# Kernel optimization log

Measured on AMD Instinct MI355X. Metric: run time of the kernel, lower is better.

The kernel has to match this reference:

```python
import jax, jax.numpy as jnp
import numpy as np

EPS_NORM = 1e-6
EPS_Q = 1e-5


def rmsnorm(x, g):
    ms = jnp.mean(x * x, axis=-1, keepdims=True)
    return x * jax.lax.rsqrt(ms + EPS_NORM) * g


def bitlinear(x, w, g):
    # RMSNorm -> absmax int8 activation quant -> absmean ternary weight quant -> matmul -> rescale
    xn = rmsnorm(x, g)
    x_scale = jnp.maximum(jnp.max(jnp.abs(xn), axis=-1, keepdims=True), EPS_Q)
    xq = jnp.clip(jnp.round(xn * 127.0 / x_scale), -128.0, 127.0)  # STE irrelevant in fwd
    w_scale = jnp.maximum(jnp.mean(jnp.abs(w)), EPS_Q)
    wq = jnp.clip(jnp.round(w / w_scale), -1.0, 1.0)
    out = jnp.einsum('btd,od->bto', xq, wq)
    return out * (w_scale * x_scale / 127.0)


def rotate_half(x):
    d = x.shape[-1] // 2
    return jnp.concatenate([-x[..., d:], x[..., :d]], axis=-1)


def apply_rope(x, cos, sin):
    # x: [B, H, T, D]; cos/sin: [T, D]
    return x * cos[None, None] + rotate_half(x) * sin[None, None]


def setup_inputs() -> dict:
    key = jax.random.key(0)
    ks = jax.random.split(key, 12)
    B, T, D, H, KV = 2, 2048, 2048, 32, 8
    hd = D // H
    bound = 1.0 / np.sqrt(D)  # ~ kaiming_uniform fan_in
    inp = {
        'x': jax.random.normal(ks[0], (B, T, D), jnp.float32),
        'cos': jax.random.uniform(ks[1], (T, hd), jnp.float32),
        'sin': jax.random.uniform(ks[2], (T, hd), jnp.float32),
        'wq': jax.random.uniform(ks[3], (H * hd, D), jnp.float32, -bound, bound),
        'wk': jax.random.uniform(ks[4], (KV * hd, D), jnp.float32, -bound, bound),
        'wv': jax.random.uniform(ks[5], (KV * hd, D), jnp.float32, -bound, bound),
        'wo': jax.random.uniform(ks[6], (D, H * hd), jnp.float32, -bound, bound),
        'gq': jnp.ones((D,), jnp.float32),
        'gk': jnp.ones((D,), jnp.float32),
        'gv': jnp.ones((D,), jnp.float32),
        'go': jnp.ones((H * hd,), jnp.float32),
    }
    return inp


def reference(x, cos, sin, wq, wk, wv, wo, gq, gk, gv, go):
    B, T, D = x.shape
    H, KV = 32, 8
    hd = D // H
    n_rep = H // KV

    q = bitlinear(x, wq, gq).reshape(B, T, H, hd).transpose(0, 2, 1, 3)   # [B,H,T,hd]
    k = bitlinear(x, wk, gk).reshape(B, T, KV, hd).transpose(0, 2, 1, 3)  # [B,KV,T,hd]
    v = bitlinear(x, wv, gv).reshape(B, T, KV, hd).transpose(0, 2, 1, 3)

    q = apply_rope(q, cos, sin)
    k = apply_rope(k, cos, sin)

    # GQA repeat_interleave on head dim
    k = jnp.repeat(k, n_rep, axis=1)  # [B,H,T,hd]
    v = jnp.repeat(v, n_rep, axis=1)

    scale = 1.0 / np.sqrt(hd)
    scores = jnp.einsum('bhqd,bhkd->bhqk', q, k) * scale
    causal = jnp.tril(jnp.ones((T, T), bool))
    scores = jnp.where(causal, scores, jnp.finfo(scores.dtype).min)
    attn = jax.nn.softmax(scores, axis=-1)
    out = jnp.einsum('bhqk,bhkd->bhqd', attn, v)
    out = out.transpose(0, 2, 1, 3).reshape(B, T, H * hd)
    return bitlinear(out, wo, go)
```

## Files before the change

### kernel.cpp

```cpp
#include <hip/hip_runtime.h>
#include <stdint.h>

constexpr int B   = 2;
constexpr int T   = 2048;
constexpr int D   = 2048;
constexpr int H   = 32;
constexpr int KVH = 8;
constexpr int HD  = 64;
constexpr int R   = B * T;
constexpr int OKV = KVH * HD;

using bf16x8 = __attribute__((ext_vector_type(8))) __bf16;
using f32x4  = __attribute__((ext_vector_type(4))) float;
using i32x4  = __attribute__((ext_vector_type(4))) int;

__device__ inline float fast_exp2(float x) {
#if __has_builtin(__builtin_amdgcn_exp2f)
    return __builtin_amdgcn_exp2f(x);
#else
    return exp2f(x);
#endif
}

__device__ inline float max3f(float a, float b, float c) {
    return fmaxf(fmaxf(a, b), c);
}

__device__ inline uint16_t f2bf(float f) {
    uint32_t u = __float_as_uint(f);
    u += 0x7fff + ((u >> 16) & 1);
    return (uint16_t)(u >> 16);
}

__device__ inline uint32_t pack_bf16(float a, float b) {
#if __has_builtin(__builtin_amdgcn_cvt_pk_bf16_f32)
    union { __attribute__((ext_vector_type(2))) __bf16 v; uint32_t u; } r;
    r.v = __builtin_amdgcn_cvt_pk_bf16_f32(a, b);
    return r.u;
#else
    return (uint32_t)f2bf(a) | ((uint32_t)f2bf(b) << 16);
#endif
}

__device__ inline void async16(const void* g, void* l) {
    __builtin_amdgcn_global_load_lds((const __attribute__((address_space(1))) unsigned int*)g,
                                     (__attribute__((address_space(3))) unsigned int*)l,
                                     16, 0, 0);
}

__global__ void absmean4_kernel(const float* __restrict__ w0, const float* __restrict__ w1,
                                const float* __restrict__ w2, const float* __restrict__ w3,
                                double* __restrict__ sums) {
    __shared__ float red[256];
    const float* ws[4] = {w0, w1, w2, w3};
    const int ns[4] = {D * D, OKV * D, OKV * D, D * D};
    int wi = blockIdx.y;
    const float* w = ws[wi];
    int n = ns[wi];
    int tid = threadIdx.x;
    float s = 0.f;
    for (int i = blockIdx.x * 256 + tid; i < n; i += gridDim.x * 256)
        s += fabsf(w[i]);
    red[tid] = s;
    __syncthreads();
    for (int st = 128; st > 0; st >>= 1) {
        if (tid < st) red[tid] += red[tid + st];
        __syncthreads();
    }
    if (tid == 0) atomicAdd(&sums[wi], (double)red[0]);
}

__global__ void quantw4_kernel(const float* __restrict__ w0, const float* __restrict__ w1,
                               const float* __restrict__ w2, const float* __restrict__ w3,
                               int8_t* __restrict__ o0, int8_t* __restrict__ o1,
                               int8_t* __restrict__ o2, int8_t* __restrict__ o3,
                               const double* __restrict__ sums) {
    const float* ws[4] = {w0, w1, w2, w3};
    int8_t* os[4] = {o0, o1, o2, o3};
    const int ns[4] = {D * D, OKV * D, OKV * D, D * D};
    int wi = blockIdx.y;
    const float* w = ws[wi];
    int8_t* o = os[wi];
    int n = ns[wi];
    float wsc = fmaxf((float)(sums[wi] / (double)n), 1e-5f);
    for (int i = blockIdx.x * 256 + threadIdx.x; i < n; i += gridDim.x * 256) {
        float q = rintf(w[i] / wsc);
        q = fminf(fmaxf(q, -1.f), 1.f);
        o[i] = (int8_t)q;
    }
}

__global__ __launch_bounds__(256) void rmsq3_kernel(const float* __restrict__ X,
        const float* __restrict__ g0, const float* __restrict__ g1, const float* __restrict__ g2,
        int8_t* __restrict__ o0, int8_t* __restrict__ o1, int8_t* __restrict__ o2,
        float* __restrict__ s0, float* __restrict__ s1, float* __restrict__ s2) {
    __shared__ float red[256];
    int row = blockIdx.x, tid = threadIdx.x;
    const float* xr = X + (size_t)row * D;
    float xv[8];
    float ss = 0.f;
#pragma unroll
    for (int i = 0; i < 8; i++) { xv[i] = xr[tid + 256 * i]; ss += xv[i] * xv[i]; }
    red[tid] = ss;
    __syncthreads();
    for (int st = 128; st > 0; st >>= 1) {
        if (tid < st) red[tid] += red[tid + st];
        __syncthreads();
    }
    float rstd = 1.0f / sqrtf(red[0] / (float)D + 1e-6f);

    const float* gs[3] = {g0, g1, g2};
    int8_t* os[3] = {o0, o1, o2};
    float* sc[3] = {s0, s1, s2};
#pragma unroll
    for (int v = 0; v < 3; v++) {
        float xn[8];
        float amax = 0.f;
#pragma unroll
        for (int i = 0; i < 8; i++) {
            xn[i] = xv[i] * rstd * gs[v][tid + 256 * i];
            amax = fmaxf(amax, fabsf(xn[i]));
        }
        __syncthreads();
        red[tid] = amax;
        __syncthreads();
        for (int st = 128; st > 0; st >>= 1) {
            if (tid < st) red[tid] = fmaxf(red[tid], red[tid + st]);
            __syncthreads();
        }
        float xsv = fmaxf(red[0], 1e-5f);
        float q127 = 127.0f / xsv;
#pragma unroll
        for (int i = 0; i < 8; i++) {
            float q = rintf(xn[i] * q127);
            q = fminf(fmaxf(q, -128.f), 127.f);
            os[v][(size_t)row * D + tid + 256 * i] = (int8_t)q;
        }
        if (tid == 0) sc[v][row] = xsv;
    }
}

__global__ __launch_bounds__(256) void rmsq_kernel(const float* __restrict__ X,
                                                   const float* __restrict__ g,
                                                   int8_t* __restrict__ Xq,
                                                   float* __restrict__ xs_out) {
    __shared__ float red[256];
    int row = blockIdx.x, tid = threadIdx.x;
    const float* xr = X + (size_t)row * D;
    float xv[8];
    float ss = 0.f;
#pragma unroll
    for (int i = 0; i < 8; i++) { xv[i] = xr[tid + 256 * i]; ss += xv[i] * xv[i]; }
    red[tid] = ss;
    __syncthreads();
    for (int st = 128; st > 0; st >>= 1) {
        if (tid < st) red[tid] += red[tid + st];
        __syncthreads();
    }
    float rstd = 1.0f / sqrtf(red[0] / (float)D + 1e-6f);

    float xn[8];
    float amax = 0.f;
#pragma unroll
    for (int i = 0; i < 8; i++) {
        xn[i] = xv[i] * rstd * g[tid + 256 * i];
        amax = fmaxf(amax, fabsf(xn[i]));
    }
    __syncthreads();
    red[tid] = amax;
    __syncthreads();
    for (int st = 128; st > 0; st >>= 1) {
        if (tid < st) red[tid] = fmaxf(red[tid], red[tid + st]);
        __syncthreads();
    }
    float xs = fmaxf(red[0], 1e-5f);
    float q127 = 127.0f / xs;
#pragma unroll
    for (int i = 0; i < 8; i++) {
        float q = rintf(xn[i] * q127);
        q = fminf(fmaxf(q, -128.f), 127.f);
        Xq[(size_t)row * D + tid + 256 * i] = (int8_t)q;
    }
    if (tid == 0) xs_out[row] = xs;
}

template<int BN, int MODE>
__global__ __launch_bounds__(512, 4) void gemm_i8_mfma(const int8_t* __restrict__ Xq,
                                                       const int8_t* __restrict__ W8,
                                                       void* __restrict__ outp,
                                                       const float* __restrict__ xs,
                                                       const double* __restrict__ wsum, int wi,
                                                       int nw, int O,
                                                       const float* __restrict__ cs,
                                                       const float* __restrict__ sn) {
    constexpr int NT = BN / 16;
    __shared__ __align__(16) uint8_t As[2][128 * 128];
    __shared__ __align__(16) uint8_t Bs[2][BN * 128];

    const int tid  = threadIdx.x;
    const int lane = tid & 63;
    const int wv   = tid >> 6;
    const int n    = lane & 15, quad = lane >> 4;
    const int row0 = blockIdx.y * 128;
    const int col0 = blockIdx.x * BN;

    i32x4 acc[NT] = {};

    auto stage = [&](int k0, int buf) {
#pragma unroll
        for (int ps = 0; ps < 2; ps++) {
            int p = ps * 512 + wv * 64 + lane;
            int r = p >> 3, s = p & 7;
            int c = s ^ (r & 7);
            async16(Xq + (size_t)(row0 + r) * D + k0 + c * 16,
                    &As[buf][(ps * 512 + wv * 64) * 16]);
        }
#pragma unroll
        for (int ps = 0; ps < BN / 64; ps++) {
            int p = ps * 512 + wv * 64 + lane;
            int r = p >> 3, s = p & 7;
            int c = s ^ (r & 7);
            async16(W8 + (size_t)(col0 + r) * D + k0 + c * 16,
                    &Bs[buf][(ps * 512 + wv * 64) * 16]);
        }
    };

    stage(0, 0);
    __syncthreads();

    for (int k0 = 0; k0 < D; k0 += 128) {
        const int cur = (k0 >> 7) & 1;
        if (k0 + 128 < D) stage(k0 + 128, cur ^ 1);
#pragma unroll
        for (int t = 0; t < 2; t++) {
            int r = wv * 16 + n;
            i32x4 af = *(const i32x4*)&As[cur][r * 128 + (((t * 4 + quad) ^ (r & 7)) * 16)];
            i32x4 bfr[NT];
#pragma unroll
            for (int nt = 0; nt < NT; nt++) {
                int rb = nt * 16 + n;
                bfr[nt] = *(const i32x4*)&Bs[cur][rb * 128 + (((t * 4 + quad) ^ (rb & 7)) * 16)];
            }
#pragma unroll
            for (int nt = 0; nt < NT; nt++)
                acc[nt] = __builtin_amdgcn_mfma_i32_16x16x64_i8(af, bfr[nt], acc[nt], 0, 0, 0);
        }
        __syncthreads();
    }

    float w = fmaxf((float)(wsum[wi] / (double)nw), 1e-5f);
#pragma unroll
    for (int r2 = 0; r2 < 4; r2++) {
        int row = row0 + wv * 16 + quad * 4 + r2;
        float f = w * xs[row] * (1.0f / 127.0f);
        if (MODE == 0) {
            float* out = (float*)outp;
#pragma unroll
            for (int nt = 0; nt < NT; nt++)
                out[(size_t)row * O + col0 + nt * 16 + n] = (float)acc[nt][r2] * f;
        } else {
            uint16_t* out = (uint16_t*)outp;
            int t = row & (T - 1);
#pragma unroll
            for (int nt = 0; nt < NT; nt++) {
                if ((nt & 3) >= 2) continue;
                int i = (nt * 16 + n) & 63;
                float a  = (float)acc[nt][r2] * f;
                float bb = (float)acc[nt + 2][r2] * f;
                float c0 = cs[t * HD + i],      s0 = sn[t * HD + i];
                float c1 = cs[t * HD + i + 32], s1 = sn[t * HD + i + 32];
                out[(size_t)row * O + col0 + nt * 16 + n]       = f2bf(a * c0 - bb * s0);
                out[(size_t)row * O + col0 + (nt + 2) * 16 + n] = f2bf(bb * c1 + a * s1);
            }
        }
    }
}

__global__ __launch_bounds__(512, 4) void gemm_kv_mfma(const int8_t* __restrict__ Xv,
                                                       const int8_t* __restrict__ Xk,
                                                       const int8_t* __restrict__ Wv8,
                                                       const int8_t* __restrict__ Wk8,
                                                       uint16_t* __restrict__ vt,
                                                       uint16_t* __restrict__ kout,
                                                       const float* __restrict__ xsv,
                                                       const float* __restrict__ xsk,
                                                       const double* __restrict__ wsum,
                                                       const float* __restrict__ cs,
                                                       const float* __restrict__ sn) {
    constexpr int BN = 64, NT = 4;
    __shared__ __align__(16) uint8_t As[2][128 * 128];
    __shared__ __align__(16) uint8_t Bs[2][BN * 128];

    const int z = blockIdx.z;
    const int8_t* Xq = z ? Xk : Xv;
    const int8_t* W8 = z ? Wk8 : Wv8;
    const float* xs  = z ? xsk : xsv;

    const int tid  = threadIdx.x;
    const int lane = tid & 63;
    const int wv   = tid >> 6;
    const int n    = lane & 15, quad = lane >> 4;
    const int row0 = blockIdx.y * 128;
    const int col0 = blockIdx.x * BN;

    i32x4 acc[NT] = {};

    auto stage = [&](int k0, int buf) {
#pragma unroll
        for (int ps = 0; ps < 2; ps++) {
            int p = ps * 512 + wv * 64 + lane;
            int r = p >> 3, s = p & 7;
            int c = s ^ (r & 7);
            async16(Xq + (size_t)(row0 + r) * D + k0 + c * 16,
                    &As[buf][(ps * 512 + wv * 64) * 16]);
        }
        {
            int p = wv * 64 + lane;
            int r = p >> 3, s = p & 7;
            int c = s ^ (r & 7);
            async16(W8 + (size_t)(col0 + r) * D + k0 + c * 16,
                    &Bs[buf][(wv * 64) * 16]);
        }
    };

    stage(0, 0);
    __syncthreads();

    for (int k0 = 0; k0 < D; k0 += 128) {
        const int cur = (k0 >> 7) & 1;
        if (k0 + 128 < D) stage(k0 + 128, cur ^ 1);
#pragma unroll
        for (int t = 0; t < 2; t++) {
            int r = wv * 16 + n;
            i32x4 af = *(const i32x4*)&As[cur][r * 128 + (((t * 4 + quad) ^ (r & 7)) * 16)];
            i32x4 bfr[NT];
#pragma unroll
            for (int nt = 0; nt < NT; nt++) {
                int rb = nt * 16 + n;
                bfr[nt] = *(const i32x4*)&Bs[cur][rb * 128 + (((t * 4 + quad) ^ (rb & 7)) * 16)];
            }
#pragma unroll
            for (int nt = 0; nt < NT; nt++)
                acc[nt] = __builtin_amdgcn_mfma_i32_16x16x64_i8(af, bfr[nt], acc[nt], 0, 0, 0);
        }
        __syncthreads();
    }

    float w = fmaxf((float)(wsum[z ? 1 : 2] / (double)(OKV * D)), 1e-5f);
    if (z == 0) {
        int rowb = row0 + wv * 16 + quad * 4;
        int bb = rowb >> 11;
        int tb = rowb & (T - 1);
        float fr[4];
#pragma unroll
        for (int r2 = 0; r2 < 4; r2++)
            fr[r2] = w * xs[rowb + r2] * (1.0f / 127.0f);
#pragma unroll
        for (int nt = 0; nt < NT; nt++) {
            int col = col0 + nt * 16 + n;
            int kvh = col >> 6, d = col & 63;
            uint2 w2;
            w2.x = pack_bf16((float)acc[nt][0] * fr[0], (float)acc[nt][1] * fr[1]);
            w2.y = pack_bf16((float)acc[nt][2] * fr[2], (float)acc[nt][3] * fr[3]);
            *(uint2*)(vt + ((size_t)(bb * KVH + kvh) * 64 + d) * T + tb) = w2;
        }
    } else {
#pragma unroll
        for (int r2 = 0; r2 < 4; r2++) {
            int row = row0 + wv * 16 + quad * 4 + r2;
            float f = w * xs[row] * (1.0f / 127.0f);
            int t = row & (T - 1);
#pragma unroll
            for (int nt = 0; nt < 2; nt++) {
                int i = (nt * 16 + n) & 63;
                float a  = (float)acc[nt][r2] * f;
                float bb = (float)acc[nt + 2][r2] * f;
                float c0 = cs[t * HD + i],      s0 = sn[t * HD + i];
                float c1 = cs[t * HD + i + 32], s1 = sn[t * HD + i + 32];
                kout[(size_t)row * OKV + col0 + nt * 16 + n]       = f2bf(a * c0 - bb * s0);
                kout[(size_t)row * OKV + col0 + (nt + 2) * 16 + n] = f2bf(bb * c1 + a * s1);
            }
        }
    }
}

__global__ __launch_bounds__(512, 4) void attn_mfma_kernel(const uint16_t* __restrict__ qh,
                                                           const uint16_t* __restrict__ kh,
                                                           const uint16_t* __restrict__ vt,
                                                           float* __restrict__ out) {
    __shared__ __align__(16) uint16_t KsB[2][64 * 64];
    __shared__ __align__(16) uint16_t VtB[2][64 * 64];
    __shared__ __align__(16) uint16_t Pw[8][16 * 72];

    const int tid  = threadIdx.x;
    const int lane = tid & 63;
    const int wv   = tid >> 6;
    const int p = blockIdx.x, h = blockIdx.y, b = blockIdx.z;
    const int kvh = h >> 2;
    const int n = lane & 15, quad = lane >> 4;
    const float SC = 0.125f * 1.44269504089f;
    const float DEFER = 44.3614f;

    int q_lo[2] = { p * 128 + wv * 16, (15 - p) * 128 + wv * 16 };

    bf16x8 qf[2][2];
#pragma unroll
    for (int i = 0; i < 2; i++) {
        const uint16_t* qp = qh + (size_t)(b * T + q_lo[i] + n) * D + h * HD + quad * 8;
        qf[i][0] = *(const bf16x8*)(qp);
        qf[i][1] = *(const bf16x8*)(qp + 32);
    }

    f32x4 o[2][4] = {};
    float ls[2] = { 0.f, 0.f };
    float m[2] = { -INFINITY, -INFINITY };

    const uint16_t* kbase = kh + (size_t)b * T * OKV + kvh * HD;
    const uint16_t* vbase = vt + (size_t)(b * KVH + kvh) * 64 * T;

    const int nch = 32 - 2 * p;

    {
        int r = tid >> 3, sl = tid & 7;
        int c = sl ^ (r & 7);
        async16(kbase + (size_t)r * OKV + c * 8, &KsB[0][wv * 512]);
        async16(vbase + (size_t)r * T + c * 8,   &VtB[0][wv * 512]);
    }
    __syncthreads();

    for (int ch = 0; ch < nch; ch++) {
        const int cur = ch & 1;
        if (ch + 1 < nch) {
            const int t1 = (ch + 1) * 64;
            int r = tid >> 3, sl = tid & 7;
            int c = sl ^ (r & 7);
            async16(kbase + (size_t)(t1 + r) * OKV + c * 8, &KsB[cur ^ 1][wv * 512]);
            async16(vbase + (size_t)r * T + t1 + c * 8,     &VtB[cur ^ 1][wv * 512]);
        }
        const int t0 = ch * 64;
        const uint16_t* Ks = KsB[cur];
        const uint16_t* Vs = VtB[cur];

#pragma unroll
        for (int i = 0; i < 2; i++) {
            if (t0 > q_lo[i] + 15) continue;
            f32x4 sv[4] = {};
            __builtin_amdgcn_s_setprio(1);
#pragma unroll
            for (int ks = 0; ks < 2; ks++)
#pragma unroll
                for (int mt = 0; mt < 4; mt++) {
                    int r = mt * 16 + n;
                    bf16x8 kfr = *(const bf16x8*)&Ks[r * 64 + (((ks * 4 + quad) ^ (n & 7)) * 8)];
                    sv[mt] = __builtin_amdgcn_mfma_f32_16x16x32_bf16(kfr, qf[i][ks], sv[mt], 0, 0, 0);
                }
            __builtin_amdgcn_s_setprio(0);

            const int qg = q_lo[i] + n;
            const bool diag = (t0 + 63 > q_lo[i]);
            if (diag) {
#pragma unroll
                for (int mt = 0; mt < 4; mt++)
#pragma unroll
                    for (int r2 = 0; r2 < 4; r2++) {
                        int kg = t0 + mt * 16 + quad * 4 + r2;
                        if (kg > qg) sv[mt][r2] = -INFINITY;
                    }
            }
            float r0 = max3f(sv[0][0], sv[0][1], sv[0][2]);
            float r1 = max3f(sv[0][3], sv[1][0], sv[1][1]);
            float r2m = max3f(sv[1][2], sv[1][3], sv[2][0]);
            float r3 = max3f(sv[2][1], sv[2][2], sv[2][3]);
            float r4 = max3f(sv[3][0], sv[3][1], sv[3][2]);
            float mloc = fmaxf(max3f(max3f(r0, r1, r2m), r3, r4), sv[3][3]);
            mloc = fmaxf(mloc, __shfl_xor(mloc, 16));
            mloc = fmaxf(mloc, __shfl_xor(mloc, 32));
            bool upd = (mloc > m[i] + DEFER);
            if (__ballot(upd)) {
                float mnew = fmaxf(m[i], mloc);
                float corr = fast_exp2((m[i] - mnew) * SC);
                m[i] = mnew;
#pragma unroll
                for (int mt = 0; mt < 4; mt++)
#pragma unroll
                    for (int r2 = 0; r2 < 4; r2++) o[i][mt][r2] *= corr;
                ls[i] *= corr;
            }
            float msc = m[i] * SC;
#pragma unroll
            for (int mt = 0; mt < 4; mt++) {
                float pv[4];
#pragma unroll
                for (int r2 = 0; r2 < 4; r2++)
                    pv[r2] = fast_exp2(__builtin_fmaf(sv[mt][r2], SC, -msc));
                ls[i] += (pv[0] + pv[1]) + (pv[2] + pv[3]);
                uint2 w2;
                w2.x = pack_bf16(pv[0], pv[1]);
                w2.y = pack_bf16(pv[2], pv[3]);
                *(uint2*)&Pw[wv][n * 72 + mt * 16 + quad * 4] = w2;
            }
            __builtin_amdgcn_s_setprio(1);
#pragma unroll
            for (int ks = 0; ks < 2; ks++) {
                bf16x8 pf = *(const bf16x8*)&Pw[wv][n * 72 + ks * 32 + quad * 8];
#pragma unroll
                for (int mt = 0; mt < 4; mt++) {
                    int r = mt * 16 + n;
                    bf16x8 vfr = *(const bf16x8*)&Vs[r * 64 + (((ks * 4 + quad) ^ (n & 7)) * 8)];
                    o[i][mt] = __builtin_amdgcn_mfma_f32_16x16x32_bf16(vfr, pf, o[i][mt], 0, 0, 0);
                }
            }
            __builtin_amdgcn_s_setprio(0);
        }
        __syncthreads();
    }

#pragma unroll
    for (int i = 0; i < 2; i++) {
        int qg = q_lo[i] + n;
        float l = ls[i];
        l += __shfl_xor(l, 16);
        l += __shfl_xor(l, 32);
        float inv = 1.0f / l;
#pragma unroll
        for (int mt = 0; mt < 4; mt++) {
            f32x4 ov;
#pragma unroll
            for (int r2 = 0; r2 < 4; r2++) ov[r2] = o[i][mt][r2] * inv;
            *(f32x4*)(out + (size_t)(b * T + qg) * D + h * HD + mt * 16 + quad * 4) = ov;
        }
    }
}

extern "C" void kernel_launch(void* const* d_in, const int* in_sizes, int n_in,
                              void* d_out, int out_size, void* d_ws, size_t ws_size,
                              hipStream_t stream) {
    const float* x   = (const float*)d_in[0];
    const float* cs  = (const float*)d_in[1];
    const float* sn  = (const float*)d_in[2];
    const float* wq  = (const float*)d_in[3];
    const float* wk  = (const float*)d_in[4];
    const float* wv  = (const float*)d_in[5];
    const float* wo  = (const float*)d_in[6];
    const float* gq  = (const float*)d_in[7];
    const float* gk  = (const float*)d_in[8];
    const float* gv  = (const float*)d_in[9];
    const float* go  = (const float*)d_in[10];
    float* out = (float*)d_out;

    uint8_t* w = (uint8_t*)d_ws;
    double* wsum  = (double*)w;
    float* xs     = (float*)(w + 256);
    size_t off = 256 + 4 * (size_t)R * 4;
    int8_t* Wq8 = (int8_t*)(w + off); off += (size_t)D * D;
    int8_t* Wk8 = (int8_t*)(w + off); off += (size_t)OKV * D;
    int8_t* Wv8 = (int8_t*)(w + off); off += (size_t)OKV * D;
    int8_t* Wo8 = (int8_t*)(w + off); off += (size_t)D * D;
    int8_t* Xq_q = (int8_t*)(w + off); off += (size_t)R * D;
    int8_t* Xq_k = (int8_t*)(w + off); off += (size_t)R * D;
    int8_t* Xq_v = (int8_t*)(w + off); off += (size_t)R * D;
    float* ab = (float*)(w + off); off += (size_t)R * D * 4;
    float* vb = (float*)(w + off); off += (size_t)R * OKV * 4;
    uint16_t* qhb = (uint16_t*)(w + off); off += (size_t)R * D * 2;
    uint16_t* vtb = (uint16_t*)vb;
    uint16_t* khb = vtb + (size_t)R * OKV;
    int8_t*   Aq8 = Xq_q;

    (void)hipMemsetAsync(wsum, 0, 64, stream);

    absmean4_kernel<<<dim3(256, 4), 256, 0, stream>>>(wq, wk, wv, wo, wsum);
    quantw4_kernel<<<dim3(1024, 4), 256, 0, stream>>>(wq, wk, wv, wo, Wq8, Wk8, Wv8, Wo8, wsum);

    rmsq3_kernel<<<R, 256, 0, stream>>>(x, gq, gk, gv, Xq_q, Xq_k, Xq_v,
                                        xs + 0 * R, xs + 1 * R, xs + 2 * R);

    gemm_i8_mfma<128, 1><<<dim3(D / 128, R / 128), 512, 0, stream>>>(
        Xq_q, Wq8, qhb, xs + 0 * R, wsum, 0, D * D, D, cs, sn);
    gemm_kv_mfma<<<dim3(OKV / 64, R / 128, 2), 512, 0, stream>>>(
        Xq_v, Xq_k, Wv8, Wk8, vtb, khb, xs + 2 * R, xs + 1 * R, wsum, cs, sn);

    attn_mfma_kernel<<<dim3(8, H, B), 512, 0, stream>>>(qhb, khb, vtb, ab);

    rmsq_kernel<<<R, 256, 0, stream>>>(ab, go, Aq8, xs + 3 * R);
    gemm_i8_mfma<128, 0><<<dim3(D / 128, R / 128), 512, 0, stream>>>(
        Aq8, Wo8, out, xs + 3 * R, wsum, 3, D * D, D, cs, sn);
}
```

Baseline: 326.9 us.

## Merge Q/K/V int8 GEMMs into one launch with 2x2 warp tiling

Replaces the separate Q and KV int8 GEMM launches with a single gemm_qkv kernel that dispatches Q, V and K tiles by blockIdx.x, and splits the output GEMM into its own gemm_o kernel. Both kernels now use 128x128 tiles where each warp computes a 32x64 sub-tile (2x4 MFMAs) instead of 16xBN, so each A and B fragment loaded from LDS feeds more MFMAs. The goals are to remove one launch, balance the small KV GEMM with Q in one grid, and cut LDS traffic per MFMA. In exchange the KV blocks now use 128-wide tiles, giving fewer blocks, and accumulator register pressure goes up.

```diff
diff --git a/kernel.cpp b/kernel.cpp
--- a/kernel.cpp
+++ b/kernel.cpp
@@ -184,27 +184,152 @@
     if (tid == 0) xs_out[row] = xs;
 }
 
-template<int BN, int MODE>
-__global__ __launch_bounds__(512, 4) void gemm_i8_mfma(const int8_t* __restrict__ Xq,
-                                                       const int8_t* __restrict__ W8,
-                                                       void* __restrict__ outp,
-                                                       const float* __restrict__ xs,
-                                                       const double* __restrict__ wsum, int wi,
-                                                       int nw, int O,
-                                                       const float* __restrict__ cs,
-                                                       const float* __restrict__ sn) {
-    constexpr int NT = BN / 16;
+
+__global__ __launch_bounds__(512, 4) void gemm_qkv(const int8_t* __restrict__ Xqq,
+                                                   const int8_t* __restrict__ Xqk,
+                                                   const int8_t* __restrict__ Xqv,
+                                                   const int8_t* __restrict__ Wq8,
+                                                   const int8_t* __restrict__ Wk8,
+                                                   const int8_t* __restrict__ Wv8,
+                                                   uint16_t* __restrict__ qout,
+                                                   uint16_t* __restrict__ kout,
+                                                   uint16_t* __restrict__ vt,
+                                                   const float* __restrict__ xs,
+                                                   const double* __restrict__ wsum,
+                                                   const float* __restrict__ cs,
+                                                   const float* __restrict__ sn) {
     __shared__ __align__(16) uint8_t As[2][128 * 128];
-    __shared__ __align__(16) uint8_t Bs[2][BN * 128];
+    __shared__ __align__(16) uint8_t Bs[2][128 * 128];
+
+    const int bx = blockIdx.x;
+    const int z  = (bx < 16) ? 0 : ((bx < 20) ? 1 : 2);
+    const int xb = (bx < 16) ? bx : ((bx - 16) & 3);
+    const int8_t* X  = (z == 0) ? Xqq : ((z == 1) ? Xqv : Xqk);
+    const int8_t* W  = (z == 0) ? Wq8 : ((z == 1) ? Wv8 : Wk8);
+    const float* xsr = (z == 0) ? xs : ((z == 1) ? xs + 2 * R : xs + R);
+    const int wi = (z == 0) ? 0 : ((z == 1) ? 2 : 1);
+    const double nw = (z == 0) ? (double)(D * D) : (double)(OKV * D);
 
     const int tid  = threadIdx.x;
     const int lane = tid & 63;
     const int wv   = tid >> 6;
+    const int rg   = wv >> 1, cg = wv & 1;
     const int n    = lane & 15, quad = lane >> 4;
     const int row0 = blockIdx.y * 128;
-    const int col0 = blockIdx.x * BN;
-
-    i32x4 acc[NT] = {};
+    const int col0 = xb * 128;
+
+    i32x4 acc[2][4] = {};
+
+    auto stage = [&](int k0, int buf) {
+#pragma unroll
+        for (int ps = 0; ps < 2; ps++) {
+            int p = ps * 512 + wv * 64 + lane;
+            int r = p >> 3, s = p & 7;
+            int c = s ^ (r & 7);
+            async16(X + (size_t)(row0 + r) * D + k0 + c * 16,
+                    &As[buf][(ps * 512 + wv * 64) * 16]);
+        }
+#pragma unroll
+        for (int ps = 0; ps < 2; ps++) {
+            int p = ps * 512 + wv * 64 + lane;
+            int r = p >> 3, s = p & 7;
+            int c = s ^ (r & 7);
+            async16(W + (size_t)(col0 + r) * D + k0 + c * 16,
+                    &Bs[buf][(ps * 512 + wv * 64) * 16]);
+        }
+    };
+
+    stage(0, 0);
+    __syncthreads();
+
+    for (int k0 = 0; k0 < D; k0 += 128) {
+        const int cur = (k0 >> 7) & 1;
+        if (k0 + 128 < D) stage(k0 + 128, cur ^ 1);
+#pragma unroll
+        for (int t = 0; t < 2; t++) {
+            i32x4 af[2], bfr[4];
+#pragma unroll
+            for (int mt = 0; mt < 2; mt++) {
+                int r = rg * 32 + mt * 16 + n;
+                af[mt] = *(const i32x4*)&As[cur][r * 128 + (((t * 4 + quad) ^ (r & 7)) * 16)];
+            }
+#pragma unroll
+            for (int nt = 0; nt < 4; nt++) {
+                int rb = cg * 64 + nt * 16 + n;
+                bfr[nt] = *(const i32x4*)&Bs[cur][rb * 128 + (((t * 4 + quad) ^ (rb & 7)) * 16)];
+            }
+#pragma unroll
+            for (int mt = 0; mt < 2; mt++)
+#pragma unroll
+                for (int nt = 0; nt < 4; nt++)
+                    acc[mt][nt] = __builtin_amdgcn_mfma_i32_16x16x64_i8(af[mt], bfr[nt], acc[mt][nt], 0, 0, 0);
+        }
+        __syncthreads();
+    }
+
+    float w = fmaxf((float)(wsum[wi] / nw), 1e-5f);
+    if (z == 1) {
+#pragma unroll
+        for (int mt = 0; mt < 2; mt++) {
+            int rowb = row0 + rg * 32 + mt * 16 + quad * 4;
+            int bb = rowb >> 11;
+            int tb = rowb & (T - 1);
+            float fr[4];
+#pragma unroll
+            for (int r2 = 0; r2 < 4; r2++)
+                fr[r2] = w * xsr[rowb + r2] * (1.0f / 127.0f);
+#pragma unroll
+            for (int nt = 0; nt < 4; nt++) {
+                int col = col0 + cg * 64 + nt * 16 + n;
+                int kvh = col >> 6, d = col & 63;
+                uint2 w2;
+                w2.x = pack_bf16((float)acc[mt][nt][0] * fr[0], (float)acc[mt][nt][1] * fr[1]);
+                w2.y = pack_bf16((float)acc[mt][nt][2] * fr[2], (float)acc[mt][nt][3] * fr[3]);
+                *(uint2*)(vt + ((size_t)(bb * KVH + kvh) * 64 + d) * T + tb) = w2;
+            }
+        }
+    } else {
+        uint16_t* out = (z == 0) ? qout : kout;
+        const int O   = (z == 0) ? D : OKV;
+#pragma unroll
+        for (int mt = 0; mt < 2; mt++) {
+#pragma unroll
+            for (int r2 = 0; r2 < 4; r2++) {
+                int row = row0 + rg * 32 + mt * 16 + quad * 4 + r2;
+                float f = w * xsr[row] * (1.0f / 127.0f);
+                int t = row & (T - 1);
+#pragma unroll
+                for (int nt = 0; nt < 2; nt++) {
+                    int i = nt * 16 + n;
+                    float a  = (float)acc[mt][nt][r2] * f;
+                    float bb = (float)acc[mt][nt + 2][r2] * f;
+                    float c0 = cs[t * HD + i],      s0 = sn[t * HD + i];
+                    float c1 = cs[t * HD + i + 32], s1 = sn[t * HD + i + 32];
+                    out[(size_t)row * O + col0 + cg * 64 + i]      = f2bf(a * c0 - bb * s0);
+                    out[(size_t)row * O + col0 + cg * 64 + i + 32] = f2bf(bb * c1 + a * s1);
+                }
+            }
+        }
+    }
+}
+
+__global__ __launch_bounds__(512, 4) void gemm_o(const int8_t* __restrict__ Xq,
+                                                 const int8_t* __restrict__ W8,
+                                                 float* __restrict__ out,
+                                                 const float* __restrict__ xs,
+                                                 const double* __restrict__ wsum) {
+    __shared__ __align__(16) uint8_t As[2][128 * 128];
+    __shared__ __align__(16) uint8_t Bs[2][128 * 128];
+
+    const int tid  = threadIdx.x;
+    const int lane = tid & 63;
+    const int wv   = tid >> 6;
+    const int rg   = wv >> 1, cg = wv & 1;
+    const int n    = lane & 15, quad = lane >> 4;
+    const int row0 = blockIdx.y * 128;
+    const int col0 = blockIdx.x * 128;
+
+    i32x4 acc[2][4] = {};
 
     auto stage = [&](int k0, int buf) {
 #pragma unroll
@@ -216,7 +341,7 @@
                     &As[buf][(ps * 512 + wv * 64) * 16]);
         }
 #pragma unroll
-        for (int ps = 0; ps < BN / 64; ps++) {
+        for (int ps = 0; ps < 2; ps++) {
             int p = ps * 512 + wv * 64 + lane;
             int r = p >> 3, s = p & 7;
             int c = s ^ (r & 7);
@@ -233,153 +358,36 @@
         if (k0 + 128 < D) stage(k0 + 128, cur ^ 1);
 #pragma unroll
         for (int t = 0; t < 2; t++) {
-            int r = wv * 16 + n;
-            i32x4 af = *(const i32x4*)&As[cur][r * 128 + (((t * 4 + quad) ^ (r & 7)) * 16)];
-            i32x4 bfr[NT];
-#pragma unroll
-            for (int nt = 0; nt < NT; nt++) {
-                int rb = nt * 16 + n;
+            i32x4 af[2], bfr[4];
+#pragma unroll
+            for (int mt = 0; mt < 2; mt++) {
+                int r = rg * 32 + mt * 16 + n;
+                af[mt] = *(const i32x4*)&As[cur][r * 128 + (((t * 4 + quad) ^ (r & 7)) * 16)];
+            }
+#pragma unroll
+            for (int nt = 0; nt < 4; nt++) {
+                int rb = cg * 64 + nt * 16 + n;
                 bfr[nt] = *(const i32x4*)&Bs[cur][rb * 128 + (((t * 4 + quad) ^ (rb & 7)) * 16)];
             }
 #pragma unroll
-            for (int nt = 0; nt < NT; nt++)
-                acc[nt] = __builtin_amdgcn_mfma_i32_16x16x64_i8(af, bfr[nt], acc[nt], 0, 0, 0);
-        }
-        __syncthreads();
-    }
-
-    float w = fmaxf((float)(wsum[wi] / (double)nw), 1e-5f);
-#pragma unroll
-    for (int r2 = 0; r2 < 4; r2++) {
-        int row = row0 + wv * 16 + quad * 4 + r2;
-        float f = w * xs[row] * (1.0f / 127.0f);
-        if (MODE == 0) {
-            float* out = (float*)outp;
-#pragma unroll
-            for (int nt = 0; nt < NT; nt++)
-                out[(size_t)row * O + col0 + nt * 16 + n] = (float)acc[nt][r2] * f;
-        } else {
-            uint16_t* out = (uint16_t*)outp;
-            int t = row & (T - 1);
-#pragma unroll
-            for (int nt = 0; nt < NT; nt++) {
-                if ((nt & 3) >= 2) continue;
-                int i = (nt * 16 + n) & 63;
-                float a  = (float)acc[nt][r2] * f;
-                float bb = (float)acc[nt + 2][r2] * f;
-                float c0 = cs[t * HD + i],      s0 = sn[t * HD + i];
-                float c1 = cs[t * HD + i + 32], s1 = sn[t * HD + i + 32];
-                out[(size_t)row * O + col0 + nt * 16 + n]       = f2bf(a * c0 - bb * s0);
-                out[(size_t)row * O + col0 + (nt + 2) * 16 + n] = f2bf(bb * c1 + a * s1);
-            }
-        }
-    }
-}
-
-__global__ __launch_bounds__(512, 4) void gemm_kv_mfma(const int8_t* __restrict__ Xv,
-                                                       const int8_t* __restrict__ Xk,
-                                                       const int8_t* __restrict__ Wv8,
-                                                       const int8_t* __restrict__ Wk8,
-                                                       uint16_t* __restrict__ vt,
-                                                       uint16_t* __restrict__ kout,
-                                                       const float* __restrict__ xsv,
-                                                       const float* __restrict__ xsk,
-                                                       const double* __restrict__ wsum,
-                                                       const float* __restrict__ cs,
-                                                       const float* __restrict__ sn) {
-    constexpr int BN = 64, NT = 4;
-    __shared__ __align__(16) uint8_t As[2][128 * 128];
-    __shared__ __align__(16) uint8_t Bs[2][BN * 128];
-
-    const int z = blockIdx.z;
-    const int8_t* Xq = z ? Xk : Xv;
-    const int8_t* W8 = z ? Wk8 : Wv8;
-    const float* xs  = z ? xsk : xsv;
-
-    const int tid  = threadIdx.x;
-    const int lane = tid & 63;
-    const int wv   = tid >> 6;
-    const int n    = lane & 15, quad = lane >> 4;
-    const int row0 = blockIdx.y * 128;
-    const int col0 = blockIdx.x * BN;
-
-    i32x4 acc[NT] = {};
-
-    auto stage = [&](int k0, int buf) {
-#pragma unroll
-        for (int ps = 0; ps < 2; ps++) {
-            int p = ps * 512 + wv * 64 + lane;
-            int r = p >> 3, s = p & 7;
-            int c = s ^ (r & 7);
-            async16(Xq + (size_t)(row0 + r) * D + k0 + c * 16,
-                    &As[buf][(ps * 512 + wv * 64) * 16]);
-        }
-        {
-            int p = wv * 64 + lane;
-            int r = p >> 3, s = p & 7;
-            int c = s ^ (r & 7);
-            async16(W8 + (size_t)(col0 + r) * D + k0 + c * 16,
-                    &Bs[buf][(wv * 64) * 16]);
-        }
-    };
-
-    stage(0, 0);
-    __syncthreads();
-
-    for (int k0 = 0; k0 < D; k0 += 128) {
-        const int cur = (k0 >> 7) & 1;
-        if (k0 + 128 < D) stage(k0 + 128, cur ^ 1);
-#pragma unroll
-        for (int t = 0; t < 2; t++) {
-            int r = wv * 16 + n;
-            i32x4 af = *(const i32x4*)&As[cur][r * 128 + (((t * 4 + quad) ^ (r & 7)) * 16)];
-            i32x4 bfr[NT];
-#pragma unroll
-            for (int nt = 0; nt < NT; nt++) {
-                int rb = nt * 16 + n;
-                bfr[nt] = *(const i32x4*)&Bs[cur][rb * 128 + (((t * 4 + quad) ^ (rb & 7)) * 16)];
-            }
-#pragma unroll
-            for (int nt = 0; nt < NT; nt++)
-                acc[nt] = __builtin_amdgcn_mfma_i32_16x16x64_i8(af, bfr[nt], acc[nt], 0, 0, 0);
-        }
-        __syncthreads();
-    }
-
-    float w = fmaxf((float)(wsum[z ? 1 : 2] / (double)(OKV * D)), 1e-5f);
-    if (z == 0) {
-        int rowb = row0 + wv * 16 + quad * 4;
-        int bb = rowb >> 11;
-        int tb = rowb & (T - 1);
-        float fr[4];
-#pragma unroll
-        for (int r2 = 0; r2 < 4; r2++)
-            fr[r2] = w * xs[rowb + r2] * (1.0f / 127.0f);
-#pragma unroll
-        for (int nt = 0; nt < NT; nt++) {
-            int col = col0 + nt * 16 + n;
-            int kvh = col >> 6, d = col & 63;
-            uint2 w2;
-            w2.x = pack_bf16((float)acc[nt][0] * fr[0], (float)acc[nt][1] * fr[1]);
-            w2.y = pack_bf16((float)acc[nt][2] * fr[2], (float)acc[nt][3] * fr[3]);
-            *(uint2*)(vt + ((size_t)(bb * KVH + kvh) * 64 + d) * T + tb) = w2;
-        }
-    } else {
+            for (int mt = 0; mt < 2; mt++)
+#pragma unroll
+                for (int nt = 0; nt < 4; nt++)
+                    acc[mt][nt] = __builtin_amdgcn_mfma_i32_16x16x64_i8(af[mt], bfr[nt], acc[mt][nt], 0, 0, 0);
+        }
+        __syncthreads();
+    }
+
+    float w = fmaxf((float)(wsum[3] / (double)(D * D)), 1e-5f);
+#pragma unroll
+    for (int mt = 0; mt < 2; mt++) {
 #pragma unroll
         for (int r2 = 0; r2 < 4; r2++) {
-            int row = row0 + wv * 16 + quad * 4 + r2;
+            int row = row0 + rg * 32 + mt * 16 + quad * 4 + r2;
             float f = w * xs[row] * (1.0f / 127.0f);
-            int t = row & (T - 1);
-#pragma unroll
-            for (int nt = 0; nt < 2; nt++) {
-                int i = (nt * 16 + n) & 63;
-                float a  = (float)acc[nt][r2] * f;
-                float bb = (float)acc[nt + 2][r2] * f;
-                float c0 = cs[t * HD + i],      s0 = sn[t * HD + i];
-                float c1 = cs[t * HD + i + 32], s1 = sn[t * HD + i + 32];
-                kout[(size_t)row * OKV + col0 + nt * 16 + n]       = f2bf(a * c0 - bb * s0);
-                kout[(size_t)row * OKV + col0 + (nt + 2) * 16 + n] = f2bf(bb * c1 + a * s1);
-            }
+#pragma unroll
+            for (int nt = 0; nt < 4; nt++)
+                out[(size_t)row * D + col0 + cg * 64 + nt * 16 + n] = (float)acc[mt][nt][r2] * f;
         }
     }
 }
@@ -574,14 +582,11 @@
     rmsq3_kernel<<<R, 256, 0, stream>>>(x, gq, gk, gv, Xq_q, Xq_k, Xq_v,
                                         xs + 0 * R, xs + 1 * R, xs + 2 * R);
 
-    gemm_i8_mfma<128, 1><<<dim3(D / 128, R / 128), 512, 0, stream>>>(
-        Xq_q, Wq8, qhb, xs + 0 * R, wsum, 0, D * D, D, cs, sn);
-    gemm_kv_mfma<<<dim3(OKV / 64, R / 128, 2), 512, 0, stream>>>(
-        Xq_v, Xq_k, Wv8, Wk8, vtb, khb, xs + 2 * R, xs + 1 * R, wsum, cs, sn);
+    gemm_qkv<<<dim3(24, R / 128), 512, 0, stream>>>(
+        Xq_q, Xq_k, Xq_v, Wq8, Wk8, Wv8, qhb, khb, vtb, xs, wsum, cs, sn);
 
     attn_mfma_kernel<<<dim3(8, H, B), 512, 0, stream>>>(qhb, khb, vtb, ab);
 
     rmsq_kernel<<<R, 256, 0, stream>>>(ab, go, Aq8, xs + 3 * R);
-    gemm_i8_mfma<128, 0><<<dim3(D / 128, R / 128), 512, 0, stream>>>(
-        Aq8, Wo8, out, xs + 3 * R, wsum, 3, D * D, D, cs, sn);
-}
+    gemm_o<<<dim3(D / 128, R / 128), 512, 0, stream>>>(Aq8, Wo8, out, xs + 3 * R, wsum);
+}
```

Result: no change. 332.0 us (+1.5%).
